# Performance work log

Hardware: AMD Instinct MI355X
Metric: run time of the kernel (lower is better)

## Reference

```python
import jax, jax.numpy as jnp
import numpy as np

LN_EPS = 1e-6          # flax nn.LayerNorm default
ATTN_EPS = 1e-9        # numerical_stabilizer default


def ln_points(x, scale, bias):
    """flax LayerNorm(reduction_axes=-2): stats over points axis, affine over feature axis."""
    mu = jnp.mean(x, axis=-2, keepdims=True)
    var = jnp.mean(jnp.square(x), axis=-2, keepdims=True) - jnp.square(mu)
    return (x - mu) * jax.lax.rsqrt(var + LN_EPS) * scale + bias


def self_attention_layer(x, wq_i, bq_i, wk_i, bk_i, wv_i, bv_i, wo_i, bo_i, ls_i, lb_i):
    # 1x1 convs == pointwise linears
    q = x @ wq_i + bq_i                                  # [B,N,C]
    k = x @ wk_i + bk_i
    v = x @ wv_i + bv_i
    attn = jnp.einsum('bmc,bnc->bmn', q, k)              # [B,M,N]
    attn = jax.nn.softmax(attn, axis=-1)
    # extra offset-attention renorm: divide by column sums (axis=1)
    attn = attn / (ATTN_EPS + jnp.sum(attn, axis=1, keepdims=True))
    # einsum '...MN,...NC->...NC' reduces M: scales v by column sums
    col = jnp.sum(attn, axis=1)                          # [B,N]
    out = col[..., None] * v                             # [B,N,C]
    out = out @ wo_i + bo_i
    out = jax.nn.relu(ln_points(out, ls_i, lb_i))
    return out + x


def setup_inputs() -> dict:
    key = jax.random.key(0)
    ks = jax.random.split(key, 16)
    B, N, IN, C, F, L = 2, 4096, 3, 256, 1024, 4
    s_in = 1.0 / np.sqrt(IN)
    s_c = 1.0 / np.sqrt(C)
    s_f = 1.0 / np.sqrt(L * C)
    return {
        'inputs': jax.random.normal(ks[0], (B, N, IN), jnp.float32),
        'w0': jax.random.normal(ks[1], (IN, C), jnp.float32) * s_in,
        'b0': jnp.zeros((C,), jnp.float32),
        'ln0_s': jnp.ones((C,), jnp.float32),
        'ln0_b': jnp.zeros((C,), jnp.float32),
        'w1': jax.random.normal(ks[2], (C, C), jnp.float32) * s_c,
        'b1': jnp.zeros((C,), jnp.float32),
        'ln1_s': jnp.ones((C,), jnp.float32),
        'ln1_b': jnp.zeros((C,), jnp.float32),
        'wq': jax.random.normal(ks[3], (L, C, C), jnp.float32) * s_c,
        'bq': jnp.zeros((L, C), jnp.float32),
        'wk': jax.random.normal(ks[4], (L, C, C), jnp.float32) * s_c,
        'bk': jnp.zeros((L, C), jnp.float32),
        'wv': jax.random.normal(ks[5], (L, C, C), jnp.float32) * s_c,
        'bv': jnp.zeros((L, C), jnp.float32),
        'wo': jax.random.normal(ks[6], (L, C, C), jnp.float32) * s_c,
        'bo': jnp.zeros((L, C), jnp.float32),
        'attn_ln_s': jnp.ones((L, C), jnp.float32),
        'attn_ln_b': jnp.zeros((L, C), jnp.float32),
        'wf': jax.random.normal(ks[7], (L * C, F), jnp.float32) * s_f,
        'bf': jnp.zeros((F,), jnp.float32),
    }


def reference(inputs, w0, b0, ln0_s, ln0_b, w1, b1, ln1_s, ln1_b,
              wq, bq, wk, bk, wv, bv, wo, bo, attn_ln_s, attn_ln_b, wf, bf):
    # pre-conv stack
    out = ln_points(inputs @ w0 + b0, ln0_s, ln0_b)
    out = ln_points(out @ w1 + b1, ln1_s, ln1_b)
    # attention stack (4 structurally identical layers, concatenated)
    attn_outs = []
    for i in range(wq.shape[0]):
        out = self_attention_layer(out, wq[i], bq[i], wk[i], bk[i],
                                   wv[i], bv[i], wo[i], bo[i],
                                   attn_ln_s[i], attn_ln_b[i])
        attn_outs.append(out)
    out = jnp.concatenate(attn_outs, axis=-1)            # [B,N,4C]
    out = out @ wf + bf                                  # [B,N,F]
    return out
```

## Files before the change

kernel.cpp:

```cpp
#include <hip/hip_runtime.h>

#define BB 2
#define NN 4096
#define CC 256
#define FF 1024
#define NLAYER 4
#define RR (BB*NN)
#define SPLIT 16
#define PSP 16
#define QKLD (3*CC)
#define NEG_BIG (-1e30f)

typedef _Float16 h16;
typedef __attribute__((ext_vector_type(8))) _Float16 half8;
typedef __attribute__((ext_vector_type(4))) float f32x4;
typedef __attribute__((ext_vector_type(16))) float f32x16;

__device__ __forceinline__ void gload16(const h16* g, h16* l) {
    __builtin_amdgcn_global_load_lds((const __attribute__((address_space(1))) void*)g,
                                     (__attribute__((address_space(3))) void*)l, 16, 0, 0);
}

template<int ROWS>
__device__ __forceinline__ void stage_rows(const h16* __restrict__ src, int ld,
    int row0, int c0, h16* lds, int tid)
{
    int w = tid >> 6;
    #pragma unroll
    for (int t = 0; t < ROWS/32; ++t) {
        int slot = t*256 + tid;
        int row = slot >> 3;
        int pp  = slot & 7;
        int piece = pp ^ (row & 7);
        gload16(src + (size_t)(row0 + row)*ld + c0 + piece*8,
                lds + (t*256 + w*64)*8);
    }
}

__device__ __forceinline__ half8 frag_ld(const h16* lds, int row, int pl) {
    return *(const half8*)(lds + row*64 + ((pl ^ (row & 7))*8));
}

__global__ __launch_bounds__(256) void pct_wtrans(const float* __restrict__ W,
    h16* __restrict__ WT, int K, int N, int dstride)
{
    __shared__ h16 t[32][33];
    const float* Wl = W + (size_t)blockIdx.z*K*N;
    h16* WTl = WT + (size_t)blockIdx.z*dstride;
    int k0 = blockIdx.x*32, n0 = blockIdx.y*32;
    int tx = threadIdx.x & 31, ty = threadIdx.x >> 5;
    #pragma unroll
    for (int i = ty; i < 32; i += 8)
        t[i][tx] = (h16)Wl[(size_t)(k0+i)*N + n0 + tx];
    __syncthreads();
    #pragma unroll
    for (int i = ty; i < 32; i += 8)
        WTl[(size_t)(n0+i)*K + k0 + tx] = t[tx][i];
}

__global__ __launch_bounds__(256) void pct_bias3(const float* __restrict__ bq,
    const float* __restrict__ bk, const float* __restrict__ bv, float* __restrict__ o)
{
    int l = blockIdx.x, c = threadIdx.x;
    o[l*QKLD + c]        = bq[l*CC + c];
    o[l*QKLD + CC + c]   = bk[l*CC + c];
    o[l*QKLD + 2*CC + c] = bv[l*CC + c];
}

__global__ __launch_bounds__(256) void pct_embed(const float* __restrict__ inp,
    const float* __restrict__ w0, const float* __restrict__ b0, h16* __restrict__ out)
{
    int r = blockIdx.x, c = threadIdx.x;
    float a0 = inp[r*3+0], a1 = inp[r*3+1], a2 = inp[r*3+2];
    out[(size_t)r*CC + c] = (h16)(b0[c] + a0*w0[c] + a1*w0[CC+c] + a2*w0[2*CC+c]);
}

__global__ __launch_bounds__(256) void pct_colstat(const h16* __restrict__ x, int ldx,
    float* __restrict__ sums)
{
    int b = blockIdx.x, blk = blockIdx.y;
    const int rows = NN / 64;
    int c = threadIdx.x;
    const h16* p = x + ((size_t)b*NN + (size_t)blk*rows)*ldx + c;
    float s1 = 0.f, s2 = 0.f;
    for (int i = 0; i < rows; ++i) { float v = (float)p[(size_t)i*ldx]; s1 += v; s2 += v*v; }
    atomicAdd(&sums[(b*CC + c)*2 + 0], s1);
    atomicAdd(&sums[(b*CC + c)*2 + 1], s2);
}

__global__ __launch_bounds__(256) void pct_lnapply(const h16* __restrict__ x, int ldx,
    const float* __restrict__ sums, const float* __restrict__ scale, const float* __restrict__ bias,
    const h16* __restrict__ res, int ldr, h16* __restrict__ out, int ldo,
    int do_relu)
{
    int r = blockIdx.x, c = threadIdx.x;
    int b = r / NN;
    float s1 = sums[(b*CC + c)*2], s2 = sums[(b*CC + c)*2 + 1];
    float mu  = s1 * (1.f/NN);
    float var = s2 * (1.f/NN) - mu*mu;
    float rstd = rsqrtf(var + 1e-6f);
    float y = ((float)x[(size_t)r*ldx + c] - mu) * rstd * scale[c] + bias[c];
    if (do_relu) y = fmaxf(y, 0.f);
    if (res) y += (float)res[(size_t)r*ldr + c];
    out[(size_t)r*ldo + c] = (h16)y;
}

template<int BN, bool OUT_F32>
__global__ __launch_bounds__(256) void pct_gemm_f16(
    const h16* __restrict__ A, int lda,
    const h16* __restrict__ WT, const float* __restrict__ bias,
    void* __restrict__ outp, int ldo, int K, const float* __restrict__ rowS)
{
    constexpr int BJ = BN/2;
    constexpr int NF = BJ/16;
    __shared__ __align__(16) h16 Asm[128*64];
    __shared__ __align__(16) h16 Bsm[BN*64];
    const int tid = threadIdx.x;
    const int lane = tid & 63, w = tid >> 6;
    const int ln = lane & 15, lq = lane >> 4;
    const int wr = w >> 1, wc = w & 1;
    const int m0 = blockIdx.x*128, n0 = blockIdx.y*BN;
    f32x4 acc[4][NF];
    #pragma unroll
    for (int i = 0; i < 4; ++i)
        #pragma unroll
        for (int j = 0; j < NF; ++j) acc[i][j] = (f32x4){0.f,0.f,0.f,0.f};
    for (int k0 = 0; k0 < K; k0 += 64) {
        stage_rows<128>(A, lda, m0, k0, Asm, tid);
        stage_rows<BN>(WT, K, n0, k0, Bsm, tid);
        __syncthreads();
        #pragma unroll
        for (int kk = 0; kk < 2; ++kk) {
            half8 af[4], bfr[NF];
            #pragma unroll
            for (int i = 0; i < 4; ++i) af[i] = frag_ld(Asm, wr*64 + i*16 + ln, kk*4 + lq);
            #pragma unroll
            for (int j = 0; j < NF; ++j) bfr[j] = frag_ld(Bsm, wc*BJ + j*16 + ln, kk*4 + lq);
            #pragma unroll
            for (int i = 0; i < 4; ++i)
                #pragma unroll
                for (int j = 0; j < NF; ++j)
                    acc[i][j] = __builtin_amdgcn_mfma_f32_16x16x32_f16(af[i], bfr[j], acc[i][j], 0, 0, 0);
        }
        __syncthreads();
    }
    #pragma unroll
    for (int j = 0; j < NF; ++j) {
        int col = n0 + wc*BJ + j*16 + ln;
        float bv = bias[col];
        #pragma unroll
        for (int i = 0; i < 4; ++i) {
            #pragma unroll
            for (int r = 0; r < 4; ++r) {
                int row = m0 + wr*64 + i*16 + lq*4 + r;
                float sc = 1.f;
                if (rowS) { float s = rowS[row]; sc = s / (1e-9f + s); }
                float v = acc[i][j][r] * sc + bv;
                if (OUT_F32) ((float*)outp)[(size_t)row*ldo + col] = v;
                else ((h16*)outp)[(size_t)row*ldo + col] = (h16)v;
            }
        }
    }
}

__global__ __launch_bounds__(256) void attn_rowstats(const h16* __restrict__ QKV,
    float2* __restrict__ part)
{
    __shared__ __align__(16) h16 Asm[128*64];
    __shared__ __align__(16) h16 Bsm[128*64];
    const int b = blockIdx.x, mt = blockIdx.y, sp = blockIdx.z;
    const int tid = threadIdx.x;
    const int lane = tid & 63, wr = tid >> 6;
    const int ln2 = lane & 31, h = lane >> 5;
    const h16* qb = QKV + (size_t)b*NN*QKLD;
    const h16* kb = qb + CC;
    const int m0 = mt*128;
    float rm[16], rs[16];
    #pragma unroll
    for (int g = 0; g < 16; ++g) { rm[g] = NEG_BIG; rs[g] = 0.f; }

    const int nbeg = sp*(NN/SPLIT);
    for (int n0 = nbeg; n0 < nbeg + NN/SPLIT; n0 += 128) {
        f32x16 acc[4];
        #pragma unroll
        for (int j = 0; j < 4; ++j) acc[j] = (f32x16)(0.f);
        #pragma unroll
        for (int c = 0; c < 4; ++c) {
            stage_rows<128>(qb, QKLD, m0, c*64, Asm, tid);
            stage_rows<128>(kb, QKLD, n0, c*64, Bsm, tid);
            __syncthreads();
            #pragma unroll
            for (int kk = 0; kk < 4; ++kk) {
                half8 af = frag_ld(Asm, wr*32 + ln2, kk*2 + h);
                #pragma unroll
                for (int j = 0; j < 4; ++j) {
                    half8 bf = frag_ld(Bsm, j*32 + ln2, kk*2 + h);
                    acc[j] = __builtin_amdgcn_mfma_f32_32x32x16_f16(af, bf, acc[j], 0, 0, 0);
                }
            }
            __syncthreads();
        }
        #pragma unroll
        for (int g = 0; g < 16; ++g) {
            float a0 = acc[0][g], a1 = acc[1][g], a2 = acc[2][g], a3 = acc[3][g];
            float tm = fmaxf(fmaxf(a0,a1), fmaxf(a2,a3));
            float m = rm[g];
            if (tm > m) { rs[g] *= __expf(m - tm); m = tm; rm[g] = tm; }
            rs[g] += __expf(a0-m) + __expf(a1-m) + __expf(a2-m) + __expf(a3-m);
        }
    }
    #pragma unroll
    for (int g = 0; g < 16; ++g) {
        float m = rm[g], s = rs[g];
        #pragma unroll
        for (int msk = 1; msk <= 16; msk <<= 1) {
            float mo = __shfl_xor(m, msk, 64);
            float so = __shfl_xor(s, msk, 64);
            float mn = fmaxf(m, mo);
            s = s*__expf(m-mn) + so*__expf(mo-mn);
            m = mn;
        }
        if (ln2 == 0) {
            int row = m0 + wr*32 + (g & 3) + 8*(g >> 2) + 4*h;
            part[((size_t)b*NN + row)*PSP + sp] = make_float2(m, s);
        }
    }
}

__global__ __launch_bounds__(256) void pct_rowcomb(const float2* __restrict__ part,
    float2* __restrict__ rstat)
{
    int idx = blockIdx.x*256 + threadIdx.x;
    const float2* p = part + (size_t)idx*PSP;
    float m = NEG_BIG;
    #pragma unroll
    for (int s = 0; s < PSP; ++s) m = fmaxf(m, p[s].x);
    float sum = 0.f;
    #pragma unroll
    for (int s = 0; s < PSP; ++s) sum += p[s].y * __expf(p[s].x - m);
    rstat[idx] = make_float2(m, 1.0f / sum);
}

__global__ __launch_bounds__(256) void attn_colsums(const h16* __restrict__ QKV,
    const float2* __restrict__ rstat, float* __restrict__ S)
{
    __shared__ __align__(16) h16 Asm[128*64];
    __shared__ __align__(16) h16 Bsm[128*64];
    const int b = blockIdx.x, nt = blockIdx.y, sp = blockIdx.z;
    const int tid = threadIdx.x;
    const int lane = tid & 63, wr = tid >> 6;
    const int ln2 = lane & 31, h = lane >> 5;
    const h16* qb = QKV + (size_t)b*NN*QKLD;
    const h16* kb = qb + CC;
    const float2* rst = rstat + (size_t)b*NN;
    const int n0 = nt*128;
    float cs[16];
    #pragma unroll
    for (int g = 0; g < 16; ++g) cs[g] = 0.f;

    const int mbeg = sp*(NN/SPLIT);
    for (int m0 = mbeg; m0 < mbeg + NN/SPLIT; m0 += 128) {
        f32x16 acc[4];
        #pragma unroll
        for (int j = 0; j < 4; ++j) acc[j] = (f32x16)(0.f);
        #pragma unroll
        for (int c = 0; c < 4; ++c) {
            stage_rows<128>(kb, QKLD, n0, c*64, Asm, tid);
            stage_rows<128>(qb, QKLD, m0, c*64, Bsm, tid);
            __syncthreads();
            #pragma unroll
            for (int kk = 0; kk < 4; ++kk) {
                half8 af = frag_ld(Asm, wr*32 + ln2, kk*2 + h);
                #pragma unroll
                for (int j = 0; j < 4; ++j) {
                    half8 bf = frag_ld(Bsm, j*32 + ln2, kk*2 + h);
                    acc[j] = __builtin_amdgcn_mfma_f32_32x32x16_f16(af, bf, acc[j], 0, 0, 0);
                }
            }
            __syncthreads();
        }
        #pragma unroll
        for (int j = 0; j < 4; ++j) {
            float2 st = rst[m0 + j*32 + ln2];
            #pragma unroll
            for (int g = 0; g < 16; ++g)
                cs[g] += __expf(acc[j][g] - st.x) * st.y;
        }
    }
    #pragma unroll
    for (int g = 0; g < 16; ++g) {
        float s = cs[g];
        #pragma unroll
        for (int msk = 1; msk <= 16; msk <<= 1)
            s += __shfl_xor(s, msk, 64);
        if (ln2 == 0) {
            int row = n0 + wr*32 + (g & 3) + 8*(g >> 2) + 4*h;
            atomicAdd(&S[(size_t)b*NN + row], s);
        }
    }
}

extern "C" void kernel_launch(void* const* d_in, const int* in_sizes, int n_in,
                              void* d_out, int out_size, void* d_ws, size_t ws_size,
                              hipStream_t stream)
{
    const float* inp  = (const float*)d_in[0];
    const float* w0   = (const float*)d_in[1];
    const float* b0   = (const float*)d_in[2];
    const float* ln0s = (const float*)d_in[3];
    const float* ln0b = (const float*)d_in[4];
    const float* w1   = (const float*)d_in[5];
    const float* b1   = (const float*)d_in[6];
    const float* ln1s = (const float*)d_in[7];
    const float* ln1b = (const float*)d_in[8];
    const float* wq   = (const float*)d_in[9];
    const float* bq   = (const float*)d_in[10];
    const float* wk   = (const float*)d_in[11];
    const float* bk   = (const float*)d_in[12];
    const float* wv   = (const float*)d_in[13];
    const float* bv   = (const float*)d_in[14];
    const float* wo   = (const float*)d_in[15];
    const float* bo   = (const float*)d_in[16];
    const float* alns = (const float*)d_in[17];
    const float* alnb = (const float*)d_in[18];
    const float* wf   = (const float*)d_in[19];
    const float* bfb  = (const float*)d_in[20];
    float* out = (float*)d_out;

    char* p = (char*)d_ws;
    auto alloc = [&](size_t bytes) { char* r = p; p += (bytes + 255) & ~255ULL; return r; };
    h16* t0    = (h16*)alloc((size_t)RR*CC*2);
    h16* t1    = (h16*)alloc((size_t)RR*CC*2);
    h16* t2    = (h16*)alloc((size_t)RR*CC*2);
    h16* x1    = (h16*)alloc((size_t)RR*CC*2);
    h16* qkv   = (h16*)alloc((size_t)RR*QKLD*2);
    h16* oh    = (h16*)alloc((size_t)RR*CC*2);
    h16* xcat  = (h16*)alloc((size_t)RR*FF*2);
    h16* w1T   = (h16*)alloc((size_t)CC*CC*2);
    h16* wqkvT = (h16*)alloc((size_t)NLAYER*QKLD*CC*2);
    h16* woT   = (h16*)alloc((size_t)NLAYER*CC*CC*2);
    h16* wfT   = (h16*)alloc((size_t)FF*FF*2);
    float* bqkv  = (float*)alloc((size_t)NLAYER*QKLD*4);
    float2* part  = (float2*)alloc((size_t)RR*PSP*8);
    float2* rstat = (float2*)alloc((size_t)RR*8);
    float* Ssum  = (float*)alloc((size_t)NLAYER*RR*4);
    float* lns   = (float*)alloc((size_t)6*BB*CC*2*4);

    dim3 blk(256);

    hipMemsetAsync(Ssum, 0, (size_t)((char*)(lns + 6*BB*CC*2) - (char*)Ssum), stream);

    pct_wtrans<<<dim3(CC/32, CC/32, 1), blk, 0, stream>>>(w1, w1T, CC, CC, CC*CC);
    pct_wtrans<<<dim3(CC/32, CC/32, NLAYER), blk, 0, stream>>>(wq, wqkvT,            CC, CC, QKLD*CC);
    pct_wtrans<<<dim3(CC/32, CC/32, NLAYER), blk, 0, stream>>>(wk, wqkvT + CC*CC,    CC, CC, QKLD*CC);
    pct_wtrans<<<dim3(CC/32, CC/32, NLAYER), blk, 0, stream>>>(wv, wqkvT + 2*CC*CC,  CC, CC, QKLD*CC);
    pct_wtrans<<<dim3(CC/32, CC/32, NLAYER), blk, 0, stream>>>(wo, woT, CC, CC, CC*CC);
    pct_wtrans<<<dim3(FF/32, FF/32, 1), blk, 0, stream>>>(wf, wfT, FF, FF, FF*FF);
    pct_bias3<<<NLAYER, blk, 0, stream>>>(bq, bk, bv, bqkv);

    pct_embed<<<RR, blk, 0, stream>>>(inp, w0, b0, t0);
    pct_colstat<<<dim3(BB,64), blk, 0, stream>>>(t0, CC, lns + 0*BB*CC*2);
    pct_lnapply<<<RR, blk, 0, stream>>>(t0, CC, lns + 0*BB*CC*2, ln0s, ln0b, nullptr, 0, t1, CC, 0);
    pct_gemm_f16<64,false><<<dim3(RR/128, CC/64), blk, 0, stream>>>(t1, CC, w1T, b1, t2, CC, CC, nullptr);
    pct_colstat<<<dim3(BB,64), blk, 0, stream>>>(t2, CC, lns + 1*BB*CC*2);
    pct_lnapply<<<RR, blk, 0, stream>>>(t2, CC, lns + 1*BB*CC*2, ln1s, ln1b, nullptr, 0, x1, CC, 0);

    const h16* xin = x1; int ldx = CC;
    for (int i = 0; i < NLAYER; ++i) {
        pct_gemm_f16<64,false><<<dim3(RR/128, QKLD/64), blk, 0, stream>>>(
            xin, ldx, wqkvT + (size_t)i*QKLD*CC, bqkv + i*QKLD, qkv, QKLD, CC, nullptr);

        attn_rowstats<<<dim3(BB, NN/128, SPLIT), blk, 0, stream>>>(qkv, part);
        pct_rowcomb<<<RR/256, blk, 0, stream>>>(part, rstat);
        attn_colsums<<<dim3(BB, NN/128, SPLIT), blk, 0, stream>>>(qkv, rstat, Ssum + (size_t)i*RR);

        pct_gemm_f16<64,false><<<dim3(RR/128, CC/64), blk, 0, stream>>>(
            qkv + 2*CC, QKLD, woT + (size_t)i*CC*CC, bo + i*CC, oh, CC, CC, Ssum + (size_t)i*RR);

        pct_colstat<<<dim3(BB,64), blk, 0, stream>>>(oh, CC, lns + (2+i)*BB*CC*2);
        pct_lnapply<<<RR, blk, 0, stream>>>(oh, CC, lns + (2+i)*BB*CC*2, alns + i*CC, alnb + i*CC,
                                            xin, ldx, xcat + i*CC, FF, 1);
        xin = xcat + i*CC; ldx = FF;
    }

    pct_gemm_f16<128,true><<<dim3(RR/128, FF/128), blk, 0, stream>>>(xcat, FF, wfT, bfb, out, FF, FF, nullptr);
}
```

Before: 612.2 us.

## Materialize fp16 tile-relative logits instead of recomputing QK^T for column sums

The attention path used to compute QK^T twice, once for row softmax stats and once for column sums. It now computes it once, stores the logits minus each 128-wide tile's row max as fp16 (a 2x4096x4096 buffer), and keeps per-tile max and sum. A combine kernel turns these into per-tile weights, and a streaming kernel sums exp(logit)*weight down the columns. This trades the second GEMM for roughly 64MB of write plus read per layer, and the fp16 rounding of the logits adds some error. The LayerNorm stats and apply kernels are also vectorized to 8 halfs per thread, with a shared-memory reduction in the stats kernel.

Measured after the change: 698.4 us. 1.14x slower.

```diff
diff --git a/kernel.cpp b/kernel.cpp
--- a/kernel.cpp
+++ b/kernel.cpp
@@ -7,7 +7,8 @@
 #define NLAYER 4
 #define RR (BB*NN)
 #define SPLIT 16
-#define PSP 16
+#define NTILES (NN/128)
+#define MSPLIT 64
 #define QKLD (3*CC)
 #define NEG_BIG (-1e30f)
 
@@ -78,14 +79,27 @@
 __global__ __launch_bounds__(256) void pct_colstat(const h16* __restrict__ x, int ldx,
     float* __restrict__ sums)
 {
+    __shared__ float red[2][8][256];
     int b = blockIdx.x, blk = blockIdx.y;
-    const int rows = NN / 64;
+    int rt = threadIdx.x >> 5;
+    int cg = (threadIdx.x & 31) * 8;
+    const h16* p = x + ((size_t)b*NN + (size_t)blk*64 + rt)*ldx + cg;
+    float s1[8] = {0,0,0,0,0,0,0,0}, s2[8] = {0,0,0,0,0,0,0,0};
+    #pragma unroll
+    for (int i = 0; i < 8; ++i) {
+        half8 v = *(const half8*)(p + (size_t)i*8*ldx);
+        #pragma unroll
+        for (int j = 0; j < 8; ++j) { float f = (float)v[j]; s1[j] += f; s2[j] += f*f; }
+    }
+    #pragma unroll
+    for (int j = 0; j < 8; ++j) { red[0][rt][cg+j] = s1[j]; red[1][rt][cg+j] = s2[j]; }
+    __syncthreads();
     int c = threadIdx.x;
-    const h16* p = x + ((size_t)b*NN + (size_t)blk*rows)*ldx + c;
-    float s1 = 0.f, s2 = 0.f;
-    for (int i = 0; i < rows; ++i) { float v = (float)p[(size_t)i*ldx]; s1 += v; s2 += v*v; }
-    atomicAdd(&sums[(b*CC + c)*2 + 0], s1);
-    atomicAdd(&sums[(b*CC + c)*2 + 1], s2);
+    float t1 = 0.f, t2 = 0.f;
+    #pragma unroll
+    for (int r = 0; r < 8; ++r) { t1 += red[0][r][c]; t2 += red[1][r][c]; }
+    atomicAdd(&sums[(b*CC + c)*2 + 0], t1);
+    atomicAdd(&sums[(b*CC + c)*2 + 1], t2);
 }
 
 __global__ __launch_bounds__(256) void pct_lnapply(const h16* __restrict__ x, int ldx,
@@ -93,16 +107,26 @@
     const h16* __restrict__ res, int ldr, h16* __restrict__ out, int ldo,
     int do_relu)
 {
-    int r = blockIdx.x, c = threadIdx.x;
+    int r = blockIdx.x*8 + (threadIdx.x >> 5);
+    int cg = (threadIdx.x & 31) * 8;
     int b = r / NN;
-    float s1 = sums[(b*CC + c)*2], s2 = sums[(b*CC + c)*2 + 1];
-    float mu  = s1 * (1.f/NN);
-    float var = s2 * (1.f/NN) - mu*mu;
-    float rstd = rsqrtf(var + 1e-6f);
-    float y = ((float)x[(size_t)r*ldx + c] - mu) * rstd * scale[c] + bias[c];
-    if (do_relu) y = fmaxf(y, 0.f);
-    if (res) y += (float)res[(size_t)r*ldr + c];
-    out[(size_t)r*ldo + c] = (h16)y;
+    half8 xv = *(const half8*)(x + (size_t)r*ldx + cg);
+    half8 rv;
+    if (res) rv = *(const half8*)(res + (size_t)r*ldr + cg);
+    half8 ov;
+    #pragma unroll
+    for (int j = 0; j < 8; ++j) {
+        int c = cg + j;
+        float s1 = sums[(b*CC + c)*2], s2 = sums[(b*CC + c)*2 + 1];
+        float mu  = s1 * (1.f/NN);
+        float var = s2 * (1.f/NN) - mu*mu;
+        float rstd = rsqrtf(var + 1e-6f);
+        float y = ((float)xv[j] - mu) * rstd * scale[c] + bias[c];
+        if (do_relu) y = fmaxf(y, 0.f);
+        if (res) y += (float)rv[j];
+        ov[j] = (h16)y;
+    }
+    *(half8*)(out + (size_t)r*ldo + cg) = ov;
 }
 
 template<int BN, bool OUT_F32>
@@ -163,11 +187,12 @@
     }
 }
 
-__global__ __launch_bounds__(256) void attn_rowstats(const h16* __restrict__ QKV,
-    float2* __restrict__ part)
-{
-    __shared__ __align__(16) h16 Asm[128*64];
-    __shared__ __align__(16) h16 Bsm[128*64];
+__global__ __launch_bounds__(256) void attn_logits(const h16* __restrict__ QKV,
+    h16* __restrict__ Lg, float2* __restrict__ tstat)
+{
+    __shared__ __align__(16) h16 smem[16384];
+    h16* Asm = smem;
+    h16* Bsm = smem + 8192;
     const int b = blockIdx.x, mt = blockIdx.y, sp = blockIdx.z;
     const int tid = threadIdx.x;
     const int lane = tid & 63, wr = tid >> 6;
@@ -175,9 +200,7 @@
     const h16* qb = QKV + (size_t)b*NN*QKLD;
     const h16* kb = qb + CC;
     const int m0 = mt*128;
-    float rm[16], rs[16];
-    #pragma unroll
-    for (int g = 0; g < 16; ++g) { rm[g] = NEG_BIG; rs[g] = 0.f; }
+    h16* Lb = Lg + (size_t)b*NN*NN;
 
     const int nbeg = sp*(NN/SPLIT);
     for (int n0 = nbeg; n0 < nbeg + NN/SPLIT; n0 += 128) {
@@ -200,104 +223,91 @@
             }
             __syncthreads();
         }
+        float tm[16], ps[16];
         #pragma unroll
         for (int g = 0; g < 16; ++g) {
-            float a0 = acc[0][g], a1 = acc[1][g], a2 = acc[2][g], a3 = acc[3][g];
-            float tm = fmaxf(fmaxf(a0,a1), fmaxf(a2,a3));
-            float m = rm[g];
-            if (tm > m) { rs[g] *= __expf(m - tm); m = tm; rm[g] = tm; }
-            rs[g] += __expf(a0-m) + __expf(a1-m) + __expf(a2-m) + __expf(a3-m);
-        }
-    }
-    #pragma unroll
-    for (int g = 0; g < 16; ++g) {
-        float m = rm[g], s = rs[g];
-        #pragma unroll
-        for (int msk = 1; msk <= 16; msk <<= 1) {
-            float mo = __shfl_xor(m, msk, 64);
-            float so = __shfl_xor(s, msk, 64);
-            float mn = fmaxf(m, mo);
-            s = s*__expf(m-mn) + so*__expf(mo-mn);
-            m = mn;
+            float t0 = fmaxf(fmaxf(acc[0][g], acc[1][g]), fmaxf(acc[2][g], acc[3][g]));
+            #pragma unroll
+            for (int msk = 1; msk <= 16; msk <<= 1)
+                t0 = fmaxf(t0, __shfl_xor(t0, msk, 64));
+            tm[g] = t0;
+        }
+        #pragma unroll
+        for (int g = 0; g < 16; ++g) {
+            int row = wr*32 + (g & 3) + 8*(g >> 2) + 4*h;
+            float s = 0.f;
+            #pragma unroll
+            for (int j = 0; j < 4; ++j) {
+                float d = acc[j][g] - tm[g];
+                s += __expf(d);
+                smem[row*128 + j*32 + ln2] = (h16)d;
+            }
+            ps[g] = s;
+        }
+        __syncthreads();
+        #pragma unroll
+        for (int it = 0; it < 8; ++it) {
+            int idx = it*256 + tid;
+            int r = idx >> 4, cg = idx & 15;
+            *(half8*)(Lb + (size_t)(m0 + r)*NN + n0 + cg*8) = *(const half8*)(smem + r*128 + cg*8);
+        }
+        #pragma unroll
+        for (int g = 0; g < 16; ++g) {
+            float s = ps[g];
+            #pragma unroll
+            for (int msk = 1; msk <= 16; msk <<= 1)
+                s += __shfl_xor(s, msk, 64);
+            ps[g] = s;
         }
         if (ln2 == 0) {
-            int row = m0 + wr*32 + (g & 3) + 8*(g >> 2) + 4*h;
-            part[((size_t)b*NN + row)*PSP + sp] = make_float2(m, s);
-        }
-    }
-}
-
-__global__ __launch_bounds__(256) void pct_rowcomb(const float2* __restrict__ part,
-    float2* __restrict__ rstat)
+            #pragma unroll
+            for (int g = 0; g < 16; ++g) {
+                int row = m0 + wr*32 + (g & 3) + 8*(g >> 2) + 4*h;
+                tstat[((size_t)b*NN + row)*NTILES + (n0 >> 7)] = make_float2(tm[g], ps[g]);
+            }
+        }
+        __syncthreads();
+    }
+}
+
+__global__ __launch_bounds__(256) void pct_tilecomb(const float2* __restrict__ tstat,
+    float* __restrict__ wout)
 {
     int idx = blockIdx.x*256 + threadIdx.x;
-    const float2* p = part + (size_t)idx*PSP;
-    float m = NEG_BIG;
-    #pragma unroll
-    for (int s = 0; s < PSP; ++s) m = fmaxf(m, p[s].x);
-    float sum = 0.f;
-    #pragma unroll
-    for (int s = 0; s < PSP; ++s) sum += p[s].y * __expf(p[s].x - m);
-    rstat[idx] = make_float2(m, 1.0f / sum);
-}
-
-__global__ __launch_bounds__(256) void attn_colsums(const h16* __restrict__ QKV,
-    const float2* __restrict__ rstat, float* __restrict__ S)
-{
-    __shared__ __align__(16) h16 Asm[128*64];
-    __shared__ __align__(16) h16 Bsm[128*64];
-    const int b = blockIdx.x, nt = blockIdx.y, sp = blockIdx.z;
+    const float2* p = tstat + (size_t)idx*NTILES;
+    float rmax = NEG_BIG;
+    #pragma unroll
+    for (int t = 0; t < NTILES; ++t) rmax = fmaxf(rmax, p[t].x);
+    float rs = 0.f;
+    #pragma unroll
+    for (int t = 0; t < NTILES; ++t) rs += p[t].y * __expf(p[t].x - rmax);
+    float inv = 1.0f / rs;
+    #pragma unroll
+    for (int t = 0; t < NTILES; ++t)
+        wout[(size_t)idx*NTILES + t] = __expf(p[t].x - rmax) * inv;
+}
+
+__global__ __launch_bounds__(256) void attn_colsum(const h16* __restrict__ Lg,
+    const float* __restrict__ w, float* __restrict__ S)
+{
+    const int b = blockIdx.x, cc = blockIdx.y, sp = blockIdx.z;
     const int tid = threadIdx.x;
-    const int lane = tid & 63, wr = tid >> 6;
-    const int ln2 = lane & 31, h = lane >> 5;
-    const h16* qb = QKV + (size_t)b*NN*QKLD;
-    const h16* kb = qb + CC;
-    const float2* rst = rstat + (size_t)b*NN;
-    const int n0 = nt*128;
-    float cs[16];
-    #pragma unroll
-    for (int g = 0; g < 16; ++g) cs[g] = 0.f;
-
-    const int mbeg = sp*(NN/SPLIT);
-    for (int m0 = mbeg; m0 < mbeg + NN/SPLIT; m0 += 128) {
-        f32x16 acc[4];
-        #pragma unroll
-        for (int j = 0; j < 4; ++j) acc[j] = (f32x16)(0.f);
-        #pragma unroll
-        for (int c = 0; c < 4; ++c) {
-            stage_rows<128>(kb, QKLD, n0, c*64, Asm, tid);
-            stage_rows<128>(qb, QKLD, m0, c*64, Bsm, tid);
-            __syncthreads();
-            #pragma unroll
-            for (int kk = 0; kk < 4; ++kk) {
-                half8 af = frag_ld(Asm, wr*32 + ln2, kk*2 + h);
-                #pragma unroll
-                for (int j = 0; j < 4; ++j) {
-                    half8 bf = frag_ld(Bsm, j*32 + ln2, kk*2 + h);
-                    acc[j] = __builtin_amdgcn_mfma_f32_32x32x16_f16(af, bf, acc[j], 0, 0, 0);
-                }
-            }
-            __syncthreads();
-        }
-        #pragma unroll
-        for (int j = 0; j < 4; ++j) {
-            float2 st = rst[m0 + j*32 + ln2];
-            #pragma unroll
-            for (int g = 0; g < 16; ++g)
-                cs[g] += __expf(acc[j][g] - st.x) * st.y;
-        }
-    }
-    #pragma unroll
-    for (int g = 0; g < 16; ++g) {
-        float s = cs[g];
-        #pragma unroll
-        for (int msk = 1; msk <= 16; msk <<= 1)
-            s += __shfl_xor(s, msk, 64);
-        if (ln2 == 0) {
-            int row = n0 + wr*32 + (g & 3) + 8*(g >> 2) + 4*h;
-            atomicAdd(&S[(size_t)b*NN + row], s);
-        }
-    }
+    const int col0 = cc*2048 + tid*8;
+    const int tile = col0 >> 7;
+    const h16* base = Lg + (size_t)b*NN*NN + col0;
+    const float* wrow = w + (size_t)b*NN*NTILES + tile;
+    float cs[8] = {0.f,0.f,0.f,0.f,0.f,0.f,0.f,0.f};
+    const int mbeg = sp*(NN/MSPLIT);
+    #pragma unroll 4
+    for (int m = mbeg; m < mbeg + NN/MSPLIT; ++m) {
+        half8 v = *(const half8*)(base + (size_t)m*NN);
+        float wv = wrow[(size_t)m*NTILES];
+        #pragma unroll
+        for (int i = 0; i < 8; ++i) cs[i] += __expf((float)v[i]) * wv;
+    }
+    #pragma unroll
+    for (int i = 0; i < 8; ++i)
+        atomicAdd(&S[(size_t)b*NN + col0 + i], cs[i]);
 }
 
 extern "C" void kernel_launch(void* const* d_in, const int* in_sizes, int n_in,
@@ -341,8 +351,9 @@
     h16* woT   = (h16*)alloc((size_t)NLAYER*CC*CC*2);
     h16* wfT   = (h16*)alloc((size_t)FF*FF*2);
     float* bqkv  = (float*)alloc((size_t)NLAYER*QKLD*4);
-    float2* part  = (float2*)alloc((size_t)RR*PSP*8);
-    float2* rstat = (float2*)alloc((size_t)RR*8);
+    h16* Lg      = (h16*)alloc((size_t)BB*NN*NN*2);
+    float2* tstat= (float2*)alloc((size_t)RR*NTILES*8);
+    float* wbuf  = (float*)alloc((size_t)RR*NTILES*4);
     float* Ssum  = (float*)alloc((size_t)NLAYER*RR*4);
     float* lns   = (float*)alloc((size_t)6*BB*CC*2*4);
 
@@ -360,26 +371,26 @@
 
     pct_embed<<<RR, blk, 0, stream>>>(inp, w0, b0, t0);
     pct_colstat<<<dim3(BB,64), blk, 0, stream>>>(t0, CC, lns + 0*BB*CC*2);
-    pct_lnapply<<<RR, blk, 0, stream>>>(t0, CC, lns + 0*BB*CC*2, ln0s, ln0b, nullptr, 0, t1, CC, 0);
+    pct_lnapply<<<RR/8, blk, 0, stream>>>(t0, CC, lns + 0*BB*CC*2, ln0s, ln0b, nullptr, 0, t1, CC, 0);
     pct_gemm_f16<64,false><<<dim3(RR/128, CC/64), blk, 0, stream>>>(t1, CC, w1T, b1, t2, CC, CC, nullptr);
     pct_colstat<<<dim3(BB,64), blk, 0, stream>>>(t2, CC, lns + 1*BB*CC*2);
-    pct_lnapply<<<RR, blk, 0, stream>>>(t2, CC, lns + 1*BB*CC*2, ln1s, ln1b, nullptr, 0, x1, CC, 0);
+    pct_lnapply<<<RR/8, blk, 0, stream>>>(t2, CC, lns + 1*BB*CC*2, ln1s, ln1b, nullptr, 0, x1, CC, 0);
 
     const h16* xin = x1; int ldx = CC;
     for (int i = 0; i < NLAYER; ++i) {
         pct_gemm_f16<64,false><<<dim3(RR/128, QKLD/64), blk, 0, stream>>>(
             xin, ldx, wqkvT + (size_t)i*QKLD*CC, bqkv + i*QKLD, qkv, QKLD, CC, nullptr);
 
-        attn_rowstats<<<dim3(BB, NN/128, SPLIT), blk, 0, stream>>>(qkv, part);
-        pct_rowcomb<<<RR/256, blk, 0, stream>>>(part, rstat);
-        attn_colsums<<<dim3(BB, NN/128, SPLIT), blk, 0, stream>>>(qkv, rstat, Ssum + (size_t)i*RR);
+        attn_logits<<<dim3(BB, NN/128, SPLIT), blk, 0, stream>>>(qkv, Lg, tstat);
+        pct_tilecomb<<<RR/256, blk, 0, stream>>>(tstat, wbuf);
+        attn_colsum<<<dim3(BB, NN/2048, MSPLIT), blk, 0, stream>>>(Lg, wbuf, Ssum + (size_t)i*RR);
 
         pct_gemm_f16<64,false><<<dim3(RR/128, CC/64), blk, 0, stream>>>(
             qkv + 2*CC, QKLD, woT + (size_t)i*CC*CC, bo + i*CC, oh, CC, CC, Ssum + (size_t)i*RR);
 
         pct_colstat<<<dim3(BB,64), blk, 0, stream>>>(oh, CC, lns + (2+i)*BB*CC*2);
-        pct_lnapply<<<RR, blk, 0, stream>>>(oh, CC, lns + (2+i)*BB*CC*2, alns + i*CC, alnb + i*CC,
-                                            xin, ldx, xcat + i*CC, FF, 1);
+        pct_lnapply<<<RR/8, blk, 0, stream>>>(oh, CC, lns + (2+i)*BB*CC*2, alns + i*CC, alnb + i*CC,
+                                              xin, ldx, xcat + i*CC, FF, 1);
         xin = xcat + i*CC; ldx = FF;
     }
 
```
